# Kernel optimization log

Hardware: AMD Instinct MI355X
Metric: run time of the kernel (lower is better)

The kernel has to match this reference:

```python
import jax, jax.numpy as jnp
import numpy as np

H = 256
L = 5
N = 50000


def setup_inputs() -> dict:
    key = jax.random.key(0)
    ks = jax.random.split(key, 12)
    E = 800000
    x = jax.random.normal(ks[0], (N, H), dtype=jnp.float32)
    edge_index = jax.random.randint(ks[1], (2, E), 0, N, dtype=jnp.int64)
    edge_weight = jax.random.uniform(ks[2], (E,), dtype=jnp.float32)
    s = 1.0 / np.sqrt(H)
    weight = jax.random.uniform(ks[3], (L, H, H), dtype=jnp.float32, minval=-s, maxval=s)
    w_ih = jax.random.uniform(ks[4], (3 * H, H), dtype=jnp.float32, minval=-s, maxval=s)
    w_hh = jax.random.uniform(ks[5], (3 * H, H), dtype=jnp.float32, minval=-s, maxval=s)
    b_ih = jax.random.uniform(ks[6], (3 * H,), dtype=jnp.float32, minval=-s, maxval=s)
    b_hh = jax.random.uniform(ks[7], (3 * H,), dtype=jnp.float32, minval=-s, maxval=s)
    fc_w = jax.random.uniform(ks[8], (1, H), dtype=jnp.float32, minval=-s, maxval=s)
    fc_b = jax.random.uniform(ks[9], (1,), dtype=jnp.float32, minval=-s, maxval=s)
    return {"x": x, "edge_index": edge_index, "edge_weight": edge_weight,
            "weight": weight, "w_ih": w_ih, "w_hh": w_hh, "b_ih": b_ih,
            "b_hh": b_hh, "fc_w": fc_w, "fc_b": fc_b, "prob": 0}


def _gru_cell(m, h, w_ih, w_hh, b_ih, b_hh):
    # PyTorch GRUCell: gates ordered (r, z, n)
    gi = m @ w_ih.T + b_ih  # [N, 3H]
    gh = h @ w_hh.T + b_hh  # [N, 3H]
    r = jax.nn.sigmoid(gi[:, :H] + gh[:, :H])
    z = jax.nn.sigmoid(gi[:, H:2 * H] + gh[:, H:2 * H])
    n = jnp.tanh(gi[:, 2 * H:] + r * gh[:, 2 * H:])
    return (1.0 - z) * n + z * h


def reference(x, edge_index, edge_weight, weight, w_ih, w_hh, b_ih, b_hh, fc_w, fc_b, prob):
    src = edge_index[0]
    dst = edge_index[1]
    h = x
    for i in range(L):
        m = h @ weight[i]                       # [N, H] per-layer linear transform
        msg = edge_weight[:, None] * m[src]     # [E, H] gather + edge weighting
        agg = jax.ops.segment_sum(msg, dst, num_segments=N)  # scatter-add
        h = _gru_cell(agg, h, w_ih, w_hh, b_ih, b_hh)
    h = jax.nn.relu(h)
    # dropout with p=prob; reference runs deterministically with p=0 (eval mode)
    out = h @ fc_w.T + fc_b                     # [N, 1]
    return out
```

## Files before the change

### kernel.cpp

```cpp
#include <hip/hip_runtime.h>
#include <hip/hip_bf16.h>
#include <math.h>


#define HDIM 256

using bf16x8 = __attribute__((ext_vector_type(8))) short;
using f32x4  = __attribute__((ext_vector_type(4))) float;

__device__ __forceinline__ bf16x8 ldfrag(const ushort* p) {
    union { uint4 u; bf16x8 f; } x;
    x.u = *(const uint4*)p;
    return x.f;
}
#define MFMA(a, b, c) __builtin_amdgcn_mfma_f32_16x16x32_bf16((a), (b), (c), 0, 0, 0)
#define GLD16(g, l)                                                            \
    __builtin_amdgcn_global_load_lds(                                          \
        (const __attribute__((address_space(1))) void*)(g),                    \
        (__attribute__((address_space(3))) void*)(l), 16, 0, 0)

__device__ __forceinline__ float ldf(const void* p, size_t i, int isbf) {
    if (isbf) return __bfloat162float(((const __hip_bfloat16*)p)[i]);
    return ((const float*)p)[i];
}
__device__ __forceinline__ ushort f2bs(float v) {
    __hip_bfloat16 b = __float2bfloat16(v);
    return *(ushort*)&b;
}
__device__ __forceinline__ float bs2f(ushort u) {
    __hip_bfloat16 b = *(__hip_bfloat16*)&u;
    return __bfloat162float(b);
}
__device__ __forceinline__ size_t taddrH(int n, int k) {
    return (size_t)(n >> 4) * 4096 + (size_t)((k >> 5) << 9)
         + (size_t)(((k >> 3) & 3) << 7) + (size_t)((n & 15) << 3) + (k & 7);
}
__device__ __forceinline__ size_t taddrA(int n, int k) {
    return (size_t)(n >> 4) * 8192 + (size_t)((k >> 5) << 9)
         + (size_t)(((k >> 3) & 3) << 7) + (size_t)((n & 15) << 3) + (k & 7);
}

__global__ void detect_k(const void* x, const void* ei, int* flags) {
    if (blockIdx.x == 0 && threadIdx.x == 0) {
        const __hip_bfloat16* xb = (const __hip_bfloat16*)x;
        int isbf = 1;
        for (int i = 0; i < 1024; ++i) {
            float v = fabsf(__bfloat162float(xb[i]));
            if (!(v < 1e6f)) { isbf = 0; break; }
        }
        flags[0] = isbf;
        const int* e32 = (const int*)ei;
        int orv = e32[1] | e32[3] | e32[5] | e32[7] | e32[9] | e32[11];
        flags[1] = (orv == 0) ? 1 : 0;
    }
}

__global__ void conv_h0_k(const void* x, ushort* HH, ushort* HL,
                          const int* flags, int useHL, int Nn, size_t npad256) {
    size_t i = (size_t)blockIdx.x * blockDim.x + threadIdx.x;
    if (i >= npad256) return;
    const int n = (int)(i >> 8), k = (int)(i & 255);
    float v = 0.f;
    if (n < Nn) v = ldf(x, i, flags[0]);
    const ushort hi = f2bs(v);
    const size_t a = taddrH(n, k);
    HH[a] = hi;
    if (useHL) HL[a] = f2bs(v - bs2f(hi));
}

__global__ void prep_k(const void* w, const void* wih, const void* whh,
                       const void* bih, const void* bhh,
                       ushort* BgH, ushort* BgL, ushort* BwH, ushort* BwL,
                       float* bsum, float* bni, float* bnh,
                       const int* flags, int L) {
    int i = blockIdx.x * blockDim.x + threadIdx.x;
    int isbf = flags[0];
    if (i < 1048576) {
        const int j = i >> 10, k = i & 1023;
        const int g = (j >> 4) & 3, b = ((j >> 6) << 4) + (j & 15);
        const int kk = k & 255, seg = k >> 8;
        float v = 0.f;
        if (g == 0) v = (seg < 2) ? ldf(wih, (size_t)b * 256 + kk, isbf)
                                  : ldf(whh, (size_t)b * 256 + kk, isbf);
        else if (g == 1) v = (seg < 2) ? ldf(wih, (size_t)(256 + b) * 256 + kk, isbf)
                                       : ldf(whh, (size_t)(256 + b) * 256 + kk, isbf);
        else if (g == 2) v = (seg < 2) ? ldf(wih, (size_t)(512 + b) * 256 + kk, isbf) : 0.f;
        else             v = (seg < 2) ? 0.f : ldf(whh, (size_t)(512 + b) * 256 + kk, isbf);
        const ushort hi = f2bs(v);
        const int ct = j >> 4, c = k >> 5;
        const size_t a = (size_t)(ct * 32 + c) * 512
                       + (size_t)(((k >> 3) & 3) << 7) + ((j & 15) << 3) + (k & 7);
        BgH[a] = hi; BgL[a] = f2bs(v - bs2f(hi));
    }
    if (i < L * 131072) {
        const int l = i >> 17, r2 = i & 131071;
        const int j = r2 >> 9, k = r2 & 511;
        const int kk = k & 255;
        const float v = ldf(w, ((size_t)l << 16) + (size_t)kk * 256 + j, isbf);
        const ushort hi = f2bs(v);
        const int ct = j >> 4, c = k >> 5;
        const size_t a = (size_t)l * 131072 + (size_t)(ct * 16 + c) * 512
                       + (size_t)(((k >> 3) & 3) << 7) + ((j & 15) << 3) + (k & 7);
        BwH[a] = hi; BwL[a] = f2bs(v - bs2f(hi));
    }
    if (i < 512) bsum[i] = ldf(bih, i, isbf) + ldf(bhh, i, isbf);
    if (i < 256) {
        bni[i] = ldf(bih, 512 + i, isbf);
        bnh[i] = ldf(bhh, 512 + i, isbf);
    }
}


__global__ void zero_int_k(int* p, int n) {
    int i = blockIdx.x * blockDim.x + threadIdx.x;
    if (i < n) p[i] = 0;
}

__global__ void count_k(const void* ei, int* cnt, const int* flags, int E) {
    int e = blockIdx.x * blockDim.x + threadIdx.x;
    if (e >= E) return;
    const int* e32 = (const int*)ei;
    int d = flags[1] ? e32[2 * ((size_t)E + e)] : e32[(size_t)E + e];
    atomicAdd(&cnt[d], 1);
}

__global__ __launch_bounds__(256)
void scan1_k(const int* cnt, int* ptr, int* bsumN, int N) {
    __shared__ int s[256];
    const int t = threadIdx.x;
    const int gid = blockIdx.x * 256 + t;
    int v = (gid < N) ? cnt[gid] : 0;
    const int own = v;
    s[t] = v;
    __syncthreads();
#pragma unroll
    for (int off = 1; off < 256; off <<= 1) {
        int add = (t >= off) ? s[t - off] : 0;
        __syncthreads();
        s[t] += add;
        __syncthreads();
    }
    if (gid < N) ptr[gid] = s[t] - own;
    if (t == 255) bsumN[blockIdx.x] = s[255];
}

__global__ __launch_bounds__(256)
void scan2_k(int* bsumN, int NB) {
    __shared__ int s[256];
    __shared__ int carry;
    const int t = threadIdx.x;
    if (t == 0) carry = 0;
    __syncthreads();
    for (int base = 0; base < NB; base += 256) {
        const int i = base + t;
        int v = (i < NB) ? bsumN[i] : 0;
        const int own = v;
        s[t] = v;
        __syncthreads();
#pragma unroll
        for (int off = 1; off < 256; off <<= 1) {
            int add = (t >= off) ? s[t - off] : 0;
            __syncthreads();
            s[t] += add;
            __syncthreads();
        }
        if (i < NB) bsumN[i] = carry + s[t] - own;
        __syncthreads();
        if (t == 0) carry += s[255];
        __syncthreads();
    }
}

__global__ void scan3_k(int* ptr, int* cursor, const int* bsumN, int N, int E) {
    const int gid = blockIdx.x * 256 + threadIdx.x;
    if (gid < N) {
        const int p = ptr[gid] + bsumN[blockIdx.x];
        ptr[gid] = p;
        cursor[gid] = p;
    }
    if (gid == 0) ptr[N] = E;
}

__global__ void fill_k(const void* ei, const void* ew, int* cursor,
                       int* srcs, float* wse, const int* flags, int E) {
    int e = blockIdx.x * blockDim.x + threadIdx.x;
    if (e >= E) return;
    const int* e32 = (const int*)ei;
    int s, d;
    if (flags[1]) { s = e32[2 * (size_t)e]; d = e32[2 * ((size_t)E + e)]; }
    else          { s = e32[e];             d = e32[(size_t)E + e]; }
    const int p = atomicAdd(&cursor[d], 1);
    srcs[p] = s;
    wse[p] = ldf(ew, e, flags[0]);
}

__global__ __launch_bounds__(256)
void spmm_k(const float* __restrict__ m, const int* __restrict__ ptr,
            const int* __restrict__ srcs, const float* __restrict__ wse,
            ushort* __restrict__ AGG, int N) {
    const int node = blockIdx.x * 4 + (threadIdx.x >> 6);
    if (node >= N) return;
    const int lane4 = (threadIdx.x & 63) << 2;
    const int p0 = ptr[node], p1 = ptr[node + 1];
    float4 acc = make_float4(0.f, 0.f, 0.f, 0.f);
    int j = p0;
    for (; j + 1 < p1; j += 2) {
        const int s0 = srcs[j], s1 = srcs[j + 1];
        const float w0 = wse[j], w1 = wse[j + 1];
        const float4 v0 = *(const float4*)&m[(size_t)s0 * HDIM + lane4];
        const float4 v1 = *(const float4*)&m[(size_t)s1 * HDIM + lane4];
        acc.x = fmaf(w0, v0.x, acc.x); acc.y = fmaf(w0, v0.y, acc.y);
        acc.z = fmaf(w0, v0.z, acc.z); acc.w = fmaf(w0, v0.w, acc.w);
        acc.x = fmaf(w1, v1.x, acc.x); acc.y = fmaf(w1, v1.y, acc.y);
        acc.z = fmaf(w1, v1.z, acc.z); acc.w = fmaf(w1, v1.w, acc.w);
    }
    if (j < p1) {
        const int s0 = srcs[j];
        const float w0 = wse[j];
        const float4 v0 = *(const float4*)&m[(size_t)s0 * HDIM + lane4];
        acc.x = fmaf(w0, v0.x, acc.x); acc.y = fmaf(w0, v0.y, acc.y);
        acc.z = fmaf(w0, v0.z, acc.z); acc.w = fmaf(w0, v0.w, acc.w);
    }
    ushort4 hi, lo;
    hi.x = f2bs(acc.x); lo.x = f2bs(acc.x - bs2f(hi.x));
    hi.y = f2bs(acc.y); lo.y = f2bs(acc.y - bs2f(hi.y));
    hi.z = f2bs(acc.z); lo.z = f2bs(acc.z - bs2f(hi.z));
    hi.w = f2bs(acc.w); lo.w = f2bs(acc.w - bs2f(hi.w));
    *(ushort4*)&AGG[taddrA(node, lane4)] = hi;
    *(ushort4*)&AGG[taddrA(node, 256 + lane4)] = lo;
}

__global__ __launch_bounds__(256)
void m_gemm_k(const ushort* __restrict__ HH, const ushort* __restrict__ HL,
              const ushort* __restrict__ BwHl, const ushort* __restrict__ BwLl,
              float* __restrict__ m, const int* __restrict__ flags,
              int useHL, int nRB) {
    __shared__ ushort lds[12288];
    const int rb = blockIdx.x >> 1, cgB = blockIdx.x & 1;
    if (rb >= nRB) return;
    const int tid = threadIdx.x, lane = tid & 63;
    const int wv = __builtin_amdgcn_readfirstlane(tid >> 6);
    const int wr = wv & 1, wc = wv >> 1;
    const int lm = lane & 15, lq = lane >> 4;
    const int fullsplit = !flags[0];
    const int rt = rb * 8, t0 = 2 * wv;
    f32x4 acc[4][4];
#pragma unroll
    for (int i = 0; i < 4; ++i)
#pragma unroll
        for (int j = 0; j < 4; ++j) acc[i][j] = (f32x4){0.f, 0.f, 0.f, 0.f};

#define MG_CHUNK(c, A0, DOLO)                                                  \
    do {                                                                       \
        __syncthreads();                                                       \
        GLD16((A0) + (size_t)lane * 8, &lds[t0 * 512]);                        \
        GLD16((A0) + 4096 + (size_t)lane * 8, &lds[t0 * 512 + 512]);           \
        const size_t bb = ((size_t)(8 * cgB + t0) * 16 + (size_t)(c)) * 512;   \
        GLD16(BwHl + bb + (size_t)lane * 8, &lds[4096 + t0 * 512]);            \
        GLD16(BwHl + bb + 8192 + (size_t)lane * 8, &lds[4096 + t0 * 512 + 512]); \
        if (DOLO) {                                                            \
            GLD16(BwLl + bb + (size_t)lane * 8, &lds[8192 + t0 * 512]);        \
            GLD16(BwLl + bb + 8192 + (size_t)lane * 8, &lds[8192 + t0 * 512 + 512]); \
        }                                                                      \
        __syncthreads();                                                       \
        bf16x8 af[4], bfh[4];                                                  \
        _Pragma("unroll")                                                      \
        for (int i = 0; i < 4; ++i)                                            \
            af[i] = ldfrag(&lds[(4 * wr + i) * 512 + lq * 128 + lm * 8]);      \
        _Pragma("unroll")                                                      \
        for (int j = 0; j < 4; ++j)                                            \
            bfh[j] = ldfrag(&lds[4096 + (4 * wc + j) * 512 + lq * 128 + lm * 8]); \
        _Pragma("unroll")                                                      \
        for (int i = 0; i < 4; ++i)                                            \
            _Pragma("unroll")                                                  \
            for (int j = 0; j < 4; ++j) acc[i][j] = MFMA(af[i], bfh[j], acc[i][j]); \
        if (DOLO) {                                                            \
            _Pragma("unroll")                                                  \
            for (int j = 0; j < 4; ++j) {                                      \
                const bf16x8 bl = ldfrag(&lds[8192 + (4 * wc + j) * 512 + lq * 128 + lm * 8]); \
                _Pragma("unroll")                                              \
                for (int i = 0; i < 4; ++i) acc[i][j] = MFMA(af[i], bl, acc[i][j]); \
            }                                                                  \
        }                                                                      \
    } while (0)

    for (int c = 0; c < 8; ++c) {
        const ushort* a0 = HH + (size_t)(rt + t0) * 4096 + (size_t)c * 512;
        MG_CHUNK(c, a0, fullsplit);
    }
    if (useHL) {
        for (int c = 8; c < 16; ++c) {
            const ushort* a0 = HL + (size_t)(rt + t0) * 4096 + (size_t)(c - 8) * 512;
            MG_CHUNK(c, a0, 0);
        }
    }
#undef MG_CHUNK

#pragma unroll
    for (int i = 0; i < 4; ++i) {
        const int row = rb * 128 + wr * 64 + i * 16 + lq * 4;
#pragma unroll
        for (int j = 0; j < 4; ++j) {
            const int col = cgB * 128 + wc * 64 + j * 16 + lm;
#pragma unroll
            for (int v = 0; v < 4; ++v)
                m[(size_t)(row + v) * 256 + col] = acc[i][j][v];
        }
    }
}

__global__ __launch_bounds__(256)
void gates_k(const ushort* __restrict__ AGG,
             const ushort* __restrict__ HH, const ushort* __restrict__ HL,
             const ushort* __restrict__ BgH, const ushort* __restrict__ BgL,
             const float* __restrict__ bsum, const float* __restrict__ bni,
             const float* __restrict__ bnh,
             ushort* __restrict__ HnH, ushort* __restrict__ HnL,
             const int* __restrict__ flags, int useHL, int nRB) {
    __shared__ ushort lds[24576];
    const int x = blockIdx.x & 7, rem = blockIdx.x >> 3;
    const int cgB = rem & 7, rbHi = rem >> 3;
    const int rb = rbHi * 8 + x;
    if (rb >= nRB) return;
    const int tid = threadIdx.x, lane = tid & 63;
    const int wv = __builtin_amdgcn_readfirstlane(tid >> 6);
    const int wr = wv & 1, wc = wv >> 1;
    const int lm = lane & 15, lq = lane >> 4;
    const int fullsplit = !flags[0];
    const int rt = rb * 8, t0 = 2 * wv;
    f32x4 acc[4][4];
#pragma unroll
    for (int i = 0; i < 4; ++i)
#pragma unroll
        for (int j = 0; j < 4; ++j) acc[i][j] = (f32x4){0.f, 0.f, 0.f, 0.f};

#define GT_STEP(c0, A0, ASTRIDE, JSKIP, DOLO)                                  \
    do {                                                                       \
        __syncthreads();                                                       \
        GLD16((A0) + (size_t)lane * 8, &lds[t0 * 512]);                        \
        GLD16((A0) + (ASTRIDE) + (size_t)lane * 8, &lds[t0 * 512 + 512]);      \
        GLD16((A0) + 512 + (size_t)lane * 8, &lds[12288 + t0 * 512]);          \
        GLD16((A0) + (ASTRIDE) + 512 + (size_t)lane * 8, &lds[12288 + t0 * 512 + 512]); \
        const size_t bb = ((size_t)(8 * cgB + t0) * 32 + (size_t)(c0)) * 512;  \
        if ((t0 & 3) != (JSKIP)) {                                             \
            GLD16(BgH + bb + (size_t)lane * 8, &lds[4096 + t0 * 512]);         \
            GLD16(BgH + bb + 512 + (size_t)lane * 8, &lds[12288 + 4096 + t0 * 512]); \
        }                                                                      \
        if (((t0 + 1) & 3) != (JSKIP)) {                                       \
            GLD16(BgH + bb + 16384 + (size_t)lane * 8, &lds[4096 + t0 * 512 + 512]); \
            GLD16(BgH + bb + 16896 + (size_t)lane * 8, &lds[12288 + 4096 + t0 * 512 + 512]); \
        }                                                                      \
        if (DOLO) {                                                            \
            if ((t0 & 3) != (JSKIP)) {                                         \
                GLD16(BgL + bb + (size_t)lane * 8, &lds[8192 + t0 * 512]);     \
                GLD16(BgL + bb + 512 + (size_t)lane * 8, &lds[12288 + 8192 + t0 * 512]); \
            }                                                                  \
            if (((t0 + 1) & 3) != (JSKIP)) {                                   \
                GLD16(BgL + bb + 16384 + (size_t)lane * 8, &lds[8192 + t0 * 512 + 512]); \
                GLD16(BgL + bb + 16896 + (size_t)lane * 8, &lds[12288 + 8192 + t0 * 512 + 512]); \
            }                                                                  \
        }                                                                      \
        __syncthreads();                                                       \
        _Pragma("unroll")                                                      \
        for (int sb = 0; sb < 2; ++sb) {                                       \
            const int lb = sb * 12288;                                         \
            bf16x8 af[4];                                                      \
            _Pragma("unroll")                                                  \
            for (int i = 0; i < 4; ++i)                                        \
                af[i] = ldfrag(&lds[lb + (4 * wr + i) * 512 + lq * 128 + lm * 8]); \
            _Pragma("unroll")                                                  \
            for (int j = 0; j < 4; ++j) {                                      \
                if (j == (JSKIP)) continue;                                    \
                const bf16x8 bj = ldfrag(&lds[lb + 4096 + (4 * wc + j) * 512 + lq * 128 + lm * 8]); \
                _Pragma("unroll")                                              \
                for (int i = 0; i < 4; ++i) acc[i][j] = MFMA(af[i], bj, acc[i][j]); \
            }                                                                  \
            if (DOLO) {                                                        \
                _Pragma("unroll")                                              \
                for (int j = 0; j < 4; ++j) {                                  \
                    if (j == (JSKIP)) continue;                                \
                    const bf16x8 bl = ldfrag(&lds[lb + 8192 + (4 * wc + j) * 512 + lq * 128 + lm * 8]); \
                    _Pragma("unroll")                                          \
                    for (int i = 0; i < 4; ++i) acc[i][j] = MFMA(af[i], bl, acc[i][j]); \
                }                                                              \
            }                                                                  \
        }                                                                      \
    } while (0)

    for (int s = 0; s < 4; ++s) {
        const ushort* a0 = AGG + (size_t)(rt + t0) * 8192 + (size_t)(2 * s) * 512;
        GT_STEP(2 * s, a0, 8192, 3, fullsplit);
    }
    for (int s = 4; s < 8; ++s) {
        const ushort* a0 = AGG + (size_t)(rt + t0) * 8192 + (size_t)(2 * s) * 512;
        GT_STEP(2 * s, a0, 8192, 3, 0);
    }
    for (int s = 8; s < 12; ++s) {
        const ushort* a0 = HH + (size_t)(rt + t0) * 4096 + (size_t)(2 * s - 16) * 512;
        GT_STEP(2 * s, a0, 4096, 2, fullsplit);
    }
    if (useHL) {
        for (int s = 12; s < 16; ++s) {
            const ushort* a0 = HL + (size_t)(rt + t0) * 4096 + (size_t)(2 * s - 24) * 512;
            GT_STEP(2 * s, a0, 4096, 2, 0);
        }
    }
#undef GT_STEP

    const int b = (2 * cgB + wc) * 16 + lm;
    const float rbias = bsum[b], zbias = bsum[256 + b];
    const float ibias = bni[b], hbias = bnh[b];
#pragma unroll
    for (int i = 0; i < 4; ++i) {
        const int row0 = rb * 128 + wr * 64 + i * 16 + lq * 4;
#pragma unroll
        for (int v = 0; v < 4; ++v) {
            const int row = row0 + v;
            const size_t ho = taddrH(row, b);
            float hold = bs2f(HH[ho]);
            if (useHL) hold += bs2f(HL[ho]);
            const float r = 1.f / (1.f + expf(-(acc[i][0][v] + rbias)));
            const float z = 1.f / (1.f + expf(-(acc[i][1][v] + zbias)));
            const float nn = tanhf(acc[i][2][v] + ibias + r * (acc[i][3][v] + hbias));
            const float hv = (1.f - z) * nn + z * hold;
            const ushort hi = f2bs(hv);
            HnH[ho] = hi;
            if (useHL) HnL[ho] = f2bs(hv - bs2f(hi));
        }
    }
}

__global__ void final_k(const ushort* __restrict__ HH, const ushort* __restrict__ HL,
                        const void* fcw, const void* fcb,
                        void* out, const int* flags, int useHL, int N) {
    const int n = blockIdx.x;
    const int t = threadIdx.x;
    const int isbf = flags[0];
    const size_t off = taddrH(n, t);
    float h = bs2f(HH[off]);
    if (useHL) h += bs2f(HL[off]);
    float v = fmaxf(h, 0.f) * ldf(fcw, t, isbf);
#pragma unroll
    for (int offx = 32; offx >= 1; offx >>= 1) v += __shfl_down(v, offx);
    __shared__ float red[4];
    if ((t & 63) == 0) red[t >> 6] = v;
    __syncthreads();
    if (t == 0) {
        const float s = red[0] + red[1] + red[2] + red[3] + ldf(fcb, 0, isbf);
        if (isbf) ((__hip_bfloat16*)out)[n] = __float2bfloat16(s);
        else      ((float*)out)[n] = s;
    }
}

extern "C" void kernel_launch(void* const* d_in, const int* in_sizes, int n_in,
                              void* d_out, int out_size, void* d_ws, size_t ws_size,
                              hipStream_t stream) {
    const int H = HDIM;
    const int N = in_sizes[0] / H;
    const int E = in_sizes[2];
    const int L = in_sizes[3] / (H * H);
    const int NB = (N + 255) / 256;
    const int nRB = (N + 127) / 128;
    const size_t NPAD = (size_t)nRB * 128;
    const size_t hHalf = NPAD * 256;
    const size_t aggHalf = NPAD * 512;

    char* p = (char*)d_ws;
    int*    flags = (int*)p;              p += 64;
    ushort* AGG  = (ushort*)p;            p += aggHalf * 2;
    ushort* HxH  = (ushort*)p;            p += hHalf * 2;
    ushort* HyH  = (ushort*)p;            p += hHalf * 2;
    float*  m    = (float*)p;             p += NPAD * 256 * 4;
    ushort* BgH  = (ushort*)p;            p += (size_t)1048576 * 2;
    ushort* BgL  = (ushort*)p;            p += (size_t)1048576 * 2;
    ushort* BwH  = (ushort*)p;            p += (size_t)L * 131072 * 2;
    ushort* BwL  = (ushort*)p;            p += (size_t)L * 131072 * 2;
    float*  bsum = (float*)p;             p += 512 * 4;
    float*  bni  = (float*)p;             p += 256 * 4;
    float*  bnh  = (float*)p;             p += 256 * 4;
    int*    ptr  = (int*)p;               p += (size_t)(N + 1) * 4;
    int*    cursor = (int*)p;             p += (size_t)N * 4;
    int*    bsumN  = (int*)p;             p += (size_t)NB * 4;
    int*    srcs   = (int*)p;             p += (size_t)E * 4;
    float*  wse    = (float*)p;           p += (size_t)E * 4;
    const size_t need_reduced = (size_t)(p - (char*)d_ws);
    ushort* HxL = (ushort*)p;
    ushort* HyL = (ushort*)(p + hHalf * 2);
    const size_t need_full = need_reduced + 2 * hHalf * 2;
    const int useHL = (ws_size >= need_full) ? 1 : 0;
    if (!useHL) { HxL = HxH; HyL = HyH; }

    detect_k<<<dim3(1), dim3(64), 0, stream>>>(d_in[0], d_in[1], flags);
    conv_h0_k<<<dim3((unsigned)NPAD), dim3(256), 0, stream>>>(
        d_in[0], HxH, HxL, flags, useHL, N, NPAD * 256);
    prep_k<<<dim3(4096), dim3(256), 0, stream>>>(
        d_in[3], d_in[4], d_in[5], d_in[6], d_in[7],
        BgH, BgL, BwH, BwL, bsum, bni, bnh, flags, L);

    zero_int_k<<<dim3(NB), dim3(256), 0, stream>>>(cursor, N);
    count_k<<<dim3((E + 255) / 256), dim3(256), 0, stream>>>(d_in[1], cursor, flags, E);
    scan1_k<<<dim3(NB), dim3(256), 0, stream>>>(cursor, ptr, bsumN, N);
    scan2_k<<<dim3(1), dim3(256), 0, stream>>>(bsumN, NB);
    scan3_k<<<dim3(NB), dim3(256), 0, stream>>>(ptr, cursor, bsumN, N, E);
    fill_k<<<dim3((E + 255) / 256), dim3(256), 0, stream>>>(
        d_in[1], d_in[2], cursor, srcs, wse, flags, E);

    const dim3 blk(256);
    const unsigned gGrid = 64u * (unsigned)((nRB + 7) / 8);
    ushort *HcH = HxH, *HcL = HxL, *HnH = HyH, *HnL = HyL;
    for (int l = 0; l < L; ++l) {
        m_gemm_k<<<dim3((unsigned)(2 * nRB)), blk, 0, stream>>>(
            HcH, HcL, BwH + (size_t)l * 131072, BwL + (size_t)l * 131072,
            m, flags, useHL, nRB);
        spmm_k<<<dim3((N + 3) / 4), blk, 0, stream>>>(m, ptr, srcs, wse, AGG, N);
        gates_k<<<dim3(gGrid), blk, 0, stream>>>(
            AGG, HcH, HcL, BgH, BgL, bsum, bni, bnh, HnH, HnL, flags, useHL, nRB);
        ushort* t;
        t = HcH; HcH = HnH; HnH = t;
        t = HcL; HcL = HnL; HnL = t;
    }
    final_k<<<dim3(N), blk, 0, stream>>>(
        HcH, HcL, d_in[8], d_in[9], d_out, flags, useHL, N);
}
```

Baseline: 1.999 ms.

## Fold per-layer weight into GRU input weights and aggregate hidden state directly

Uses associativity: A·(h·W_l)·W_ihᵀ equals (A·h)·(W_l·W_ihᵀ). A small prep kernel precomputes the combined per-layer weight products once, and the per-layer m_gemm kernel is removed. The sparse aggregation now gathers the hidden state itself, stored in a packed hi/lo bf16 linear buffer that gates_k writes alongside its tiled output. This removes five dense N×256×256 split-precision GEMMs. In exchange it adds an extra hidden-state write per layer, more weight storage, and a slightly different rounding path.

```diff
diff --git a/kernel.cpp b/kernel.cpp
--- a/kernel.cpp
+++ b/kernel.cpp
@@ -30,6 +30,14 @@
 __device__ __forceinline__ float bs2f(ushort u) {
     __hip_bfloat16 b = *(__hip_bfloat16*)&u;
     return __bfloat162float(b);
+}
+__device__ __forceinline__ float unpk(uint u) {
+    return __uint_as_float(u << 16) + __uint_as_float(u & 0xffff0000u);
+}
+__device__ __forceinline__ uint pk(float v) {
+    const ushort hi = f2bs(v);
+    const ushort lo = f2bs(v - bs2f(hi));
+    return (uint)hi | ((uint)lo << 16);
 }
 __device__ __forceinline__ size_t taddrH(int n, int k) {
     return (size_t)(n >> 4) * 4096 + (size_t)((k >> 5) << 9)
@@ -55,7 +63,7 @@
     }
 }
 
-__global__ void conv_h0_k(const void* x, ushort* HH, ushort* HL,
+__global__ void conv_h0_k(const void* x, ushort* HH, ushort* HL, uint* hlin,
                           const int* flags, int useHL, int Nn, size_t npad256) {
     size_t i = (size_t)blockIdx.x * blockDim.x + threadIdx.x;
     if (i >= npad256) return;
@@ -66,42 +74,62 @@
     const size_t a = taddrH(n, k);
     HH[a] = hi;
     if (useHL) HL[a] = f2bs(v - bs2f(hi));
-}
-
-__global__ void prep_k(const void* w, const void* wih, const void* whh,
-                       const void* bih, const void* bhh,
-                       ushort* BgH, ushort* BgL, ushort* BwH, ushort* BwL,
-                       float* bsum, float* bni, float* bnh,
-                       const int* flags, int L) {
-    int i = blockIdx.x * blockDim.x + threadIdx.x;
-    int isbf = flags[0];
-    if (i < 1048576) {
-        const int j = i >> 10, k = i & 1023;
+    hlin[i] = (uint)hi | ((uint)f2bs(v - bs2f(hi)) << 16);
+}
+
+__global__ __launch_bounds__(256)
+void prep1_k(const void* wih, const void* w, float* wihp, const int* flags) {
+    __shared__ float As[16][260], Bs[16][260];
+    const int bx = blockIdx.x;
+    const int l = bx / 768, rem = bx % 768;
+    const int rt = (rem >> 4) << 4, kt = (rem & 15) << 4;
+    const int tid = threadIdx.x, isbf = flags[0];
+    for (int idx = tid; idx < 4096; idx += 256) {
+        const int row = idx >> 8, col = idx & 255;
+        As[row][col] = ldf(wih, (size_t)(rt + row) * 256 + col, isbf);
+        Bs[row][col] = ldf(w, (size_t)l * 65536 + (size_t)(kt + row) * 256 + col, isbf);
+    }
+    __syncthreads();
+    const int ri = tid >> 4, ki = tid & 15;
+    float acc = 0.f;
+    for (int j = 0; j < 256; ++j) acc = fmaf(As[ri][j], Bs[ki][j], acc);
+    wihp[((size_t)l * 768 + rt + ri) * 256 + kt + ki] = acc;
+}
+
+__global__ void prep2_k(const float* __restrict__ wihp, const void* whh,
+                        const void* bih, const void* bhh,
+                        ushort* BgAH, ushort* BgAL, ushort* BgBH, ushort* BgBL,
+                        float* bsum, float* bni, float* bnh,
+                        const int* flags, int L) {
+    const int i = blockIdx.x * blockDim.x + threadIdx.x;
+    const int isbf = flags[0];
+    if (i < (L << 19)) {
+        const int l = i >> 19, r2 = i & 524287;
+        const int j = r2 >> 9, k = r2 & 511;
         const int g = (j >> 4) & 3, b = ((j >> 6) << 4) + (j & 15);
-        const int kk = k & 255, seg = k >> 8;
-        float v = 0.f;
-        if (g == 0) v = (seg < 2) ? ldf(wih, (size_t)b * 256 + kk, isbf)
-                                  : ldf(whh, (size_t)b * 256 + kk, isbf);
-        else if (g == 1) v = (seg < 2) ? ldf(wih, (size_t)(256 + b) * 256 + kk, isbf)
-                                       : ldf(whh, (size_t)(256 + b) * 256 + kk, isbf);
-        else if (g == 2) v = (seg < 2) ? ldf(wih, (size_t)(512 + b) * 256 + kk, isbf) : 0.f;
-        else             v = (seg < 2) ? 0.f : ldf(whh, (size_t)(512 + b) * 256 + kk, isbf);
+        const int kk = k & 255;
+        const float v = (g == 3) ? 0.f
+                      : wihp[((size_t)l * 768 + g * 256 + b) * 256 + kk];
         const ushort hi = f2bs(v);
         const int ct = j >> 4, c = k >> 5;
-        const size_t a = (size_t)(ct * 32 + c) * 512
+        const size_t a = (size_t)l * 524288 + (size_t)(ct * 16 + c) * 512
                        + (size_t)(((k >> 3) & 3) << 7) + ((j & 15) << 3) + (k & 7);
-        BgH[a] = hi; BgL[a] = f2bs(v - bs2f(hi));
-    }
-    if (i < L * 131072) {
-        const int l = i >> 17, r2 = i & 131071;
-        const int j = r2 >> 9, k = r2 & 511;
+        BgAH[a] = hi; BgAL[a] = f2bs(v - bs2f(hi));
+    }
+    if (i < 524288) {
+        const int j = i >> 9, k = i & 511;
+        const int g = (j >> 4) & 3, b = ((j >> 6) << 4) + (j & 15);
         const int kk = k & 255;
-        const float v = ldf(w, ((size_t)l << 16) + (size_t)kk * 256 + j, isbf);
+        float v;
+        if (g == 0)      v = ldf(whh, (size_t)b * 256 + kk, isbf);
+        else if (g == 1) v = ldf(whh, (size_t)(256 + b) * 256 + kk, isbf);
+        else if (g == 2) v = 0.f;
+        else             v = ldf(whh, (size_t)(512 + b) * 256 + kk, isbf);
         const ushort hi = f2bs(v);
         const int ct = j >> 4, c = k >> 5;
-        const size_t a = (size_t)l * 131072 + (size_t)(ct * 16 + c) * 512
+        const size_t a = (size_t)(ct * 16 + c) * 512
                        + (size_t)(((k >> 3) & 3) << 7) + ((j & 15) << 3) + (k & 7);
-        BwH[a] = hi; BwL[a] = f2bs(v - bs2f(hi));
+        BgBH[a] = hi; BgBL[a] = f2bs(v - bs2f(hi));
     }
     if (i < 512) bsum[i] = ldf(bih, i, isbf) + ldf(bhh, i, isbf);
     if (i < 256) {
@@ -195,31 +223,33 @@
 }
 
 __global__ __launch_bounds__(256)
-void spmm_k(const float* __restrict__ m, const int* __restrict__ ptr,
+void spmm_k(const uint* __restrict__ hlin, const int* __restrict__ ptr,
             const int* __restrict__ srcs, const float* __restrict__ wse,
             ushort* __restrict__ AGG, int N) {
     const int node = blockIdx.x * 4 + (threadIdx.x >> 6);
     if (node >= N) return;
-    const int lane4 = (threadIdx.x & 63) << 2;
+    const int lane = threadIdx.x & 63;
+    const int lane4 = lane << 2;
+    const uint4* hl = (const uint4*)hlin;
     const int p0 = ptr[node], p1 = ptr[node + 1];
     float4 acc = make_float4(0.f, 0.f, 0.f, 0.f);
     int j = p0;
     for (; j + 1 < p1; j += 2) {
         const int s0 = srcs[j], s1 = srcs[j + 1];
         const float w0 = wse[j], w1 = wse[j + 1];
-        const float4 v0 = *(const float4*)&m[(size_t)s0 * HDIM + lane4];
-        const float4 v1 = *(const float4*)&m[(size_t)s1 * HDIM + lane4];
-        acc.x = fmaf(w0, v0.x, acc.x); acc.y = fmaf(w0, v0.y, acc.y);
-        acc.z = fmaf(w0, v0.z, acc.z); acc.w = fmaf(w0, v0.w, acc.w);
-        acc.x = fmaf(w1, v1.x, acc.x); acc.y = fmaf(w1, v1.y, acc.y);
-        acc.z = fmaf(w1, v1.z, acc.z); acc.w = fmaf(w1, v1.w, acc.w);
+        const uint4 u0 = hl[(size_t)s0 * 64 + lane];
+        const uint4 u1 = hl[(size_t)s1 * 64 + lane];
+        acc.x = fmaf(w0, unpk(u0.x), acc.x); acc.y = fmaf(w0, unpk(u0.y), acc.y);
+        acc.z = fmaf(w0, unpk(u0.z), acc.z); acc.w = fmaf(w0, unpk(u0.w), acc.w);
+        acc.x = fmaf(w1, unpk(u1.x), acc.x); acc.y = fmaf(w1, unpk(u1.y), acc.y);
+        acc.z = fmaf(w1, unpk(u1.z), acc.z); acc.w = fmaf(w1, unpk(u1.w), acc.w);
     }
     if (j < p1) {
         const int s0 = srcs[j];
         const float w0 = wse[j];
-        const float4 v0 = *(const float4*)&m[(size_t)s0 * HDIM + lane4];
-        acc.x = fmaf(w0, v0.x, acc.x); acc.y = fmaf(w0, v0.y, acc.y);
-        acc.z = fmaf(w0, v0.z, acc.z); acc.w = fmaf(w0, v0.w, acc.w);
+        const uint4 u0 = hl[(size_t)s0 * 64 + lane];
+        acc.x = fmaf(w0, unpk(u0.x), acc.x); acc.y = fmaf(w0, unpk(u0.y), acc.y);
+        acc.z = fmaf(w0, unpk(u0.z), acc.z); acc.w = fmaf(w0, unpk(u0.w), acc.w);
     }
     ushort4 hi, lo;
     hi.x = f2bs(acc.x); lo.x = f2bs(acc.x - bs2f(hi.x));
@@ -231,91 +261,14 @@
 }
 
 __global__ __launch_bounds__(256)
-void m_gemm_k(const ushort* __restrict__ HH, const ushort* __restrict__ HL,
-              const ushort* __restrict__ BwHl, const ushort* __restrict__ BwLl,
-              float* __restrict__ m, const int* __restrict__ flags,
-              int useHL, int nRB) {
-    __shared__ ushort lds[12288];
-    const int rb = blockIdx.x >> 1, cgB = blockIdx.x & 1;
-    if (rb >= nRB) return;
-    const int tid = threadIdx.x, lane = tid & 63;
-    const int wv = __builtin_amdgcn_readfirstlane(tid >> 6);
-    const int wr = wv & 1, wc = wv >> 1;
-    const int lm = lane & 15, lq = lane >> 4;
-    const int fullsplit = !flags[0];
-    const int rt = rb * 8, t0 = 2 * wv;
-    f32x4 acc[4][4];
-#pragma unroll
-    for (int i = 0; i < 4; ++i)
-#pragma unroll
-        for (int j = 0; j < 4; ++j) acc[i][j] = (f32x4){0.f, 0.f, 0.f, 0.f};
-
-#define MG_CHUNK(c, A0, DOLO)                                                  \
-    do {                                                                       \
-        __syncthreads();                                                       \
-        GLD16((A0) + (size_t)lane * 8, &lds[t0 * 512]);                        \
-        GLD16((A0) + 4096 + (size_t)lane * 8, &lds[t0 * 512 + 512]);           \
-        const size_t bb = ((size_t)(8 * cgB + t0) * 16 + (size_t)(c)) * 512;   \
-        GLD16(BwHl + bb + (size_t)lane * 8, &lds[4096 + t0 * 512]);            \
-        GLD16(BwHl + bb + 8192 + (size_t)lane * 8, &lds[4096 + t0 * 512 + 512]); \
-        if (DOLO) {                                                            \
-            GLD16(BwLl + bb + (size_t)lane * 8, &lds[8192 + t0 * 512]);        \
-            GLD16(BwLl + bb + 8192 + (size_t)lane * 8, &lds[8192 + t0 * 512 + 512]); \
-        }                                                                      \
-        __syncthreads();                                                       \
-        bf16x8 af[4], bfh[4];                                                  \
-        _Pragma("unroll")                                                      \
-        for (int i = 0; i < 4; ++i)                                            \
-            af[i] = ldfrag(&lds[(4 * wr + i) * 512 + lq * 128 + lm * 8]);      \
-        _Pragma("unroll")                                                      \
-        for (int j = 0; j < 4; ++j)                                            \
-            bfh[j] = ldfrag(&lds[4096 + (4 * wc + j) * 512 + lq * 128 + lm * 8]); \
-        _Pragma("unroll")                                                      \
-        for (int i = 0; i < 4; ++i)                                            \
-            _Pragma("unroll")                                                  \
-            for (int j = 0; j < 4; ++j) acc[i][j] = MFMA(af[i], bfh[j], acc[i][j]); \
-        if (DOLO) {                                                            \
-            _Pragma("unroll")                                                  \
-            for (int j = 0; j < 4; ++j) {                                      \
-                const bf16x8 bl = ldfrag(&lds[8192 + (4 * wc + j) * 512 + lq * 128 + lm * 8]); \
-                _Pragma("unroll")                                              \
-                for (int i = 0; i < 4; ++i) acc[i][j] = MFMA(af[i], bl, acc[i][j]); \
-            }                                                                  \
-        }                                                                      \
-    } while (0)
-
-    for (int c = 0; c < 8; ++c) {
-        const ushort* a0 = HH + (size_t)(rt + t0) * 4096 + (size_t)c * 512;
-        MG_CHUNK(c, a0, fullsplit);
-    }
-    if (useHL) {
-        for (int c = 8; c < 16; ++c) {
-            const ushort* a0 = HL + (size_t)(rt + t0) * 4096 + (size_t)(c - 8) * 512;
-            MG_CHUNK(c, a0, 0);
-        }
-    }
-#undef MG_CHUNK
-
-#pragma unroll
-    for (int i = 0; i < 4; ++i) {
-        const int row = rb * 128 + wr * 64 + i * 16 + lq * 4;
-#pragma unroll
-        for (int j = 0; j < 4; ++j) {
-            const int col = cgB * 128 + wc * 64 + j * 16 + lm;
-#pragma unroll
-            for (int v = 0; v < 4; ++v)
-                m[(size_t)(row + v) * 256 + col] = acc[i][j][v];
-        }
-    }
-}
-
-__global__ __launch_bounds__(256)
 void gates_k(const ushort* __restrict__ AGG,
              const ushort* __restrict__ HH, const ushort* __restrict__ HL,
-             const ushort* __restrict__ BgH, const ushort* __restrict__ BgL,
+             const ushort* __restrict__ BgAH, const ushort* __restrict__ BgAL,
+             const ushort* __restrict__ BgBH, const ushort* __restrict__ BgBL,
              const float* __restrict__ bsum, const float* __restrict__ bni,
              const float* __restrict__ bnh,
              ushort* __restrict__ HnH, ushort* __restrict__ HnL,
+             uint* __restrict__ hlin,
              const int* __restrict__ flags, int useHL, int nRB) {
     __shared__ ushort lds[24576];
     const int x = blockIdx.x & 7, rem = blockIdx.x >> 3;
@@ -334,30 +287,30 @@
 #pragma unroll
         for (int j = 0; j < 4; ++j) acc[i][j] = (f32x4){0.f, 0.f, 0.f, 0.f};
 
-#define GT_STEP(c0, A0, ASTRIDE, JSKIP, DOLO)                                  \
+#define GT_STEP(BH, BL, c0l, A0, ASTRIDE, JSKIP, DOLO)                         \
     do {                                                                       \
         __syncthreads();                                                       \
         GLD16((A0) + (size_t)lane * 8, &lds[t0 * 512]);                        \
         GLD16((A0) + (ASTRIDE) + (size_t)lane * 8, &lds[t0 * 512 + 512]);      \
         GLD16((A0) + 512 + (size_t)lane * 8, &lds[12288 + t0 * 512]);          \
         GLD16((A0) + (ASTRIDE) + 512 + (size_t)lane * 8, &lds[12288 + t0 * 512 + 512]); \
-        const size_t bb = ((size_t)(8 * cgB + t0) * 32 + (size_t)(c0)) * 512;  \
+        const size_t bb = ((size_t)(8 * cgB + t0) * 16 + (size_t)(c0l)) * 512; \
         if ((t0 & 3) != (JSKIP)) {                                             \
-            GLD16(BgH + bb + (size_t)lane * 8, &lds[4096 + t0 * 512]);         \
-            GLD16(BgH + bb + 512 + (size_t)lane * 8, &lds[12288 + 4096 + t0 * 512]); \
+            GLD16((BH) + bb + (size_t)lane * 8, &lds[4096 + t0 * 512]);        \
+            GLD16((BH) + bb + 512 + (size_t)lane * 8, &lds[12288 + 4096 + t0 * 512]); \
         }                                                                      \
         if (((t0 + 1) & 3) != (JSKIP)) {                                       \
-            GLD16(BgH + bb + 16384 + (size_t)lane * 8, &lds[4096 + t0 * 512 + 512]); \
-            GLD16(BgH + bb + 16896 + (size_t)lane * 8, &lds[12288 + 4096 + t0 * 512 + 512]); \
+            GLD16((BH) + bb + 8192 + (size_t)lane * 8, &lds[4096 + t0 * 512 + 512]); \
+            GLD16((BH) + bb + 8704 + (size_t)lane * 8, &lds[12288 + 4096 + t0 * 512 + 512]); \
         }                                                                      \
         if (DOLO) {                                                            \
             if ((t0 & 3) != (JSKIP)) {                                         \
-                GLD16(BgL + bb + (size_t)lane * 8, &lds[8192 + t0 * 512]);     \
-                GLD16(BgL + bb + 512 + (size_t)lane * 8, &lds[12288 + 8192 + t0 * 512]); \
+                GLD16((BL) + bb + (size_t)lane * 8, &lds[8192 + t0 * 512]);    \
+                GLD16((BL) + bb + 512 + (size_t)lane * 8, &lds[12288 + 8192 + t0 * 512]); \
             }                                                                  \
             if (((t0 + 1) & 3) != (JSKIP)) {                                   \
-                GLD16(BgL + bb + 16384 + (size_t)lane * 8, &lds[8192 + t0 * 512 + 512]); \
-                GLD16(BgL + bb + 16896 + (size_t)lane * 8, &lds[12288 + 8192 + t0 * 512 + 512]); \
+                GLD16((BL) + bb + 8192 + (size_t)lane * 8, &lds[8192 + t0 * 512 + 512]); \
+                GLD16((BL) + bb + 8704 + (size_t)lane * 8, &lds[12288 + 8192 + t0 * 512 + 512]); \
             }                                                                  \
         }                                                                      \
         __syncthreads();                                                       \
@@ -389,20 +342,20 @@
 
     for (int s = 0; s < 4; ++s) {
         const ushort* a0 = AGG + (size_t)(rt + t0) * 8192 + (size_t)(2 * s) * 512;
-        GT_STEP(2 * s, a0, 8192, 3, fullsplit);
+        GT_STEP(BgAH, BgAL, 2 * s, a0, 8192, 3, fullsplit);
     }
     for (int s = 4; s < 8; ++s) {
         const ushort* a0 = AGG + (size_t)(rt + t0) * 8192 + (size_t)(2 * s) * 512;
-        GT_STEP(2 * s, a0, 8192, 3, 0);
+        GT_STEP(BgAH, BgAL, 2 * s, a0, 8192, 3, 0);
     }
     for (int s = 8; s < 12; ++s) {
         const ushort* a0 = HH + (size_t)(rt + t0) * 4096 + (size_t)(2 * s - 16) * 512;
-        GT_STEP(2 * s, a0, 4096, 2, fullsplit);
+        GT_STEP(BgBH, BgBL, 2 * s - 16, a0, 4096, 2, fullsplit);
     }
     if (useHL) {
         for (int s = 12; s < 16; ++s) {
             const ushort* a0 = HL + (size_t)(rt + t0) * 4096 + (size_t)(2 * s - 24) * 512;
-            GT_STEP(2 * s, a0, 4096, 2, 0);
+            GT_STEP(BgBH, BgBL, 2 * s - 16, a0, 4096, 2, 0);
         }
     }
 #undef GT_STEP
@@ -426,6 +379,7 @@
             const ushort hi = f2bs(hv);
             HnH[ho] = hi;
             if (useHL) HnL[ho] = f2bs(hv - bs2f(hi));
+            hlin[(size_t)row * 256 + b] = (uint)hi | ((uint)f2bs(hv - bs2f(hi)) << 16);
         }
     }
 }
@@ -470,11 +424,12 @@
     ushort* AGG  = (ushort*)p;            p += aggHalf * 2;
     ushort* HxH  = (ushort*)p;            p += hHalf * 2;
     ushort* HyH  = (ushort*)p;            p += hHalf * 2;
-    float*  m    = (float*)p;             p += NPAD * 256 * 4;
-    ushort* BgH  = (ushort*)p;            p += (size_t)1048576 * 2;
-    ushort* BgL  = (ushort*)p;            p += (size_t)1048576 * 2;
-    ushort* BwH  = (ushort*)p;            p += (size_t)L * 131072 * 2;
-    ushort* BwL  = (ushort*)p;            p += (size_t)L * 131072 * 2;
+    uint*   hlin = (uint*)p;              p += NPAD * 256 * 4;
+    float*  wihp = (float*)p;             p += (size_t)L * 768 * 256 * 4;
+    ushort* BgAH = (ushort*)p;            p += (size_t)L * 524288 * 2;
+    ushort* BgAL = (ushort*)p;            p += (size_t)L * 524288 * 2;
+    ushort* BgBH = (ushort*)p;            p += (size_t)524288 * 2;
+    ushort* BgBL = (ushort*)p;            p += (size_t)524288 * 2;
     float*  bsum = (float*)p;             p += 512 * 4;
     float*  bni  = (float*)p;             p += 256 * 4;
     float*  bnh  = (float*)p;             p += 256 * 4;
@@ -492,10 +447,12 @@
 
     detect_k<<<dim3(1), dim3(64), 0, stream>>>(d_in[0], d_in[1], flags);
     conv_h0_k<<<dim3((unsigned)NPAD), dim3(256), 0, stream>>>(
-        d_in[0], HxH, HxL, flags, useHL, N, NPAD * 256);
-    prep_k<<<dim3(4096), dim3(256), 0, stream>>>(
-        d_in[3], d_in[4], d_in[5], d_in[6], d_in[7],
-        BgH, BgL, BwH, BwL, bsum, bni, bnh, flags, L);
+        d_in[0], HxH, HxL, hlin, flags, useHL, N, NPAD * 256);
+    prep1_k<<<dim3((unsigned)(L * 768)), dim3(256), 0, stream>>>(
+        d_in[4], d_in[3], wihp, flags);
+    prep2_k<<<dim3((unsigned)(L * 2048)), dim3(256), 0, stream>>>(
+        wihp, d_in[5], d_in[6], d_in[7],
+        BgAH, BgAL, BgBH, BgBL, bsum, bni, bnh, flags, L);
 
     zero_int_k<<<dim3(NB), dim3(256), 0, stream>>>(cursor, N);
     count_k<<<dim3((E + 255) / 256), dim3(256), 0, stream>>>(d_in[1], cursor, flags, E);
@@ -509,12 +466,11 @@
     const unsigned gGrid = 64u * (unsigned)((nRB + 7) / 8);
     ushort *HcH = HxH, *HcL = HxL, *HnH = HyH, *HnL = HyL;
     for (int l = 0; l < L; ++l) {
-        m_gemm_k<<<dim3((unsigned)(2 * nRB)), blk, 0, stream>>>(
-            HcH, HcL, BwH + (size_t)l * 131072, BwL + (size_t)l * 131072,
-            m, flags, useHL, nRB);
-        spmm_k<<<dim3((N + 3) / 4), blk, 0, stream>>>(m, ptr, srcs, wse, AGG, N);
+        spmm_k<<<dim3((N + 3) / 4), blk, 0, stream>>>(hlin, ptr, srcs, wse, AGG, N);
         gates_k<<<dim3(gGrid), blk, 0, stream>>>(
-            AGG, HcH, HcL, BgH, BgL, bsum, bni, bnh, HnH, HnL, flags, useHL, nRB);
+            AGG, HcH, HcL,
+            BgAH + (size_t)l * 524288, BgAL + (size_t)l * 524288,
+            BgBH, BgBL, bsum, bni, bnh, HnH, HnL, hlin, flags, useHL, nRB);
         ushort* t;
         t = HcH; HcH = HnH; HnH = t;
         t = HcL; HcL = HnL; HnL = t;
```

Result: faster. 1.884 ms (-5.7%).
